# Optimization experiments

Measured on AMD Instinct MI355X. Metric: run time of the kernel, lower is better.

Reference implementation:

```python
import jax, jax.numpy as jnp
import numpy as np

B, N, C, D = 32, 4096, 16, 256

def setup_inputs() -> dict:
    key = jax.random.key(0)
    k1, k2 = jax.random.split(key)
    r_tensor = jax.random.uniform(k1, (B, N, C), dtype=jnp.float32)
    v_tensor = jax.random.normal(k2, (B, N, D), dtype=jnp.float32)
    return {"r_tensor": r_tensor, "v_tensor": v_tensor}

def reference(r_tensor, v_tensor):
    n = r_tensor.shape[1]
    mask_belong = r_tensor >= 0.5  # (B,N,C)
    # mean over N of v[:, :, None, :] * mask[..., None]  ==  mask^T @ v / N, no (B,N,C,D) intermediate
    interest_category_mean = jnp.einsum(
        'bnc,bnd->bcd', mask_belong.astype(v_tensor.dtype), v_tensor) / n  # (B,C,D)
    mask_all_below = jnp.logical_not(mask_belong).all(axis=2)  # (B,N)
    interest_special_mean = jnp.einsum(
        'bn,bnd->bd', mask_all_below.astype(v_tensor.dtype), v_tensor) / n  # (B,D)
    v_fusion = jnp.concatenate(
        [interest_category_mean, interest_special_mean[:, None, :]], axis=1)  # (B,C+1,D)
    v_fusion = jnp.where(jnp.isnan(v_fusion), jnp.zeros((), v_fusion.dtype), v_fusion)
    return v_fusion
```

## Files before the change

kernel.cpp:

```cpp
#include <hip/hip_runtime.h>

#define B_ 32
#define N_ 4096
#define C_ 16
#define D_ 256
#define NSPLIT 64
#define ROWS (N_ / NSPLIT)
#define RPW  (ROWS / 4)
#define NG   (RPW / 4)

__global__ __launch_bounds__(256, 4)
void tensor_fusion_kernel(const float* __restrict__ r,
                          const float* __restrict__ v,
                          float* __restrict__ out) {
    const int b     = blockIdx.x >> 6;
    const int chunk = blockIdx.x & (NSPLIT - 1);
    const int tid   = threadIdx.x;
    const int wave  = tid >> 6;
    const int lane  = tid & 63;
    const int d4    = lane << 2;

    const float* __restrict__ rb = r + (size_t)b * N_ * C_;
    const float* __restrict__ vp = v + (size_t)b * N_ * D_;
    const float scale = 1.0f / (float)N_;
    float* __restrict__ ob = out + (size_t)b * 17 * D_;

    float4 acc[16];
#pragma unroll
    for (int c = 0; c < 16; ++c) acc[c] = make_float4(0.f, 0.f, 0.f, 0.f);

    const int base = chunk * ROWS + wave * RPW;

    const float* __restrict__ rptr = rb + (size_t)base * C_ + lane;
    const float* __restrict__ vptr = vp + (size_t)base * D_ + d4;

    float  rv;
    float4 v0, v1, v2, v3;
    float  rv_n;
    float4 n0, n1, n2, n3;

#define LOADG(off, RV, A, Bq, Cq, Dq)                                   \
    {                                                                   \
        RV = rptr[(size_t)(off) * C_];                                  \
        const float* _vn = vptr + (size_t)(off) * D_;                   \
        A  = *(const float4*)(_vn + 0 * D_);                            \
        Bq = *(const float4*)(_vn + 1 * D_);                            \
        Cq = *(const float4*)(_vn + 2 * D_);                            \
        Dq = *(const float4*)(_vn + 3 * D_);                            \
    }

#define ACCROW(VV, MASK)                                                \
    {                                                                   \
        const unsigned _m = (MASK);                                     \
        _Pragma("unroll")                                               \
        for (int c = 0; c < 16; ++c) {                                  \
            const float m = (_m & (1u << c)) ? 1.0f : 0.0f;             \
            acc[c].x += (VV).x * m;                                     \
            acc[c].y += (VV).y * m;                                     \
            acc[c].z += (VV).z * m;                                     \
            acc[c].w += (VV).w * m;                                     \
        }                                                               \
        if (_m == 0u) {    \
            atomicAdd(&ob[16 * D_ + d4 + 0], (VV).x * scale);           \
            atomicAdd(&ob[16 * D_ + d4 + 1], (VV).y * scale);           \
            atomicAdd(&ob[16 * D_ + d4 + 2], (VV).z * scale);           \
            atomicAdd(&ob[16 * D_ + d4 + 3], (VV).w * scale);           \
        }                                                               \
    }

    LOADG(0, rv, v0, v1, v2, v3);

#pragma unroll
    for (int g = 0; g < NG; ++g) {
        if (g + 1 < NG) LOADG((g + 1) * 4, rv_n, n0, n1, n2, n3);

        const unsigned long long bal = __ballot(rv >= 0.5f);
        ACCROW(v0, (unsigned)(bal       ) & 0xFFFFu);
        ACCROW(v1, (unsigned)(bal >> 16 ) & 0xFFFFu);
        ACCROW(v2, (unsigned)(bal >> 32 ) & 0xFFFFu);
        ACCROW(v3, (unsigned)(bal >> 48 ) & 0xFFFFu);

        if (g + 1 < NG) { rv = rv_n; v0 = n0; v1 = n1; v2 = n2; v3 = n3; }
    }

    __shared__ float4 lds4[16 * 64];
    if (wave == 0) {
#pragma unroll
        for (int c = 0; c < 16; ++c) lds4[c * 64 + lane] = acc[c];
    }
    __syncthreads();
    for (int w = 1; w < 4; ++w) {
        if (wave == w) {
#pragma unroll
            for (int c = 0; c < 16; ++c) {
                float4 t = lds4[c * 64 + lane];
                t.x += acc[c].x; t.y += acc[c].y;
                t.z += acc[c].z; t.w += acc[c].w;
                lds4[c * 64 + lane] = t;
            }
        }
        __syncthreads();
    }

    const float* lf = (const float*)lds4;
#pragma unroll
    for (int c = 0; c < 16; ++c) {
        atomicAdd(&ob[c * D_ + tid], lf[c * 256 + tid] * scale);
    }
}

extern "C" void kernel_launch(void* const* d_in, const int* in_sizes, int n_in,
                              void* d_out, int out_size, void* d_ws, size_t ws_size,
                              hipStream_t stream) {
    const float* r = (const float*)d_in[0];
    const float* v = (const float*)d_in[1];
    float* out = (float*)d_out;

    hipMemsetAsync(out, 0, (size_t)out_size * sizeof(float), stream);

    dim3 grid(B_ * NSPLIT);
    tensor_fusion_kernel<<<grid, 256, 0, stream>>>(r, v, out);
}
```

Measured before the change: 203.4 us.

## Split D across wave pairs with float2 accumulators to cut registers

Each pair of waves now splits the 256-wide D dimension in halves with float2 loads and 16 float2 accumulators instead of float4, and two wave pairs each handle 32 rows of the 64-row chunk. This halves accumulator registers, permitting launch_bounds occupancy of 8 blocks per CU, and shrinks the cross-wave LDS reduction to a single add step with fewer barriers. The cost is redundant ballot/r loads per wave pair, narrower global loads, and twice as many per-element atomics for the special row.

```diff
diff --git a/kernel.cpp b/kernel.cpp
--- a/kernel.cpp
+++ b/kernel.cpp
@@ -5,11 +5,11 @@
 #define C_ 16
 #define D_ 256
 #define NSPLIT 64
-#define ROWS (N_ / NSPLIT)
-#define RPW  (ROWS / 4)
-#define NG   (RPW / 4)
+#define ROWS 64
+#define RPS  32
+#define NG   8
 
-__global__ __launch_bounds__(256, 4)
+__global__ __launch_bounds__(256, 8)
 void tensor_fusion_kernel(const float* __restrict__ r,
                           const float* __restrict__ v,
                           float* __restrict__ out) {
@@ -18,54 +18,49 @@
     const int tid   = threadIdx.x;
     const int wave  = tid >> 6;
     const int lane  = tid & 63;
-    const int d4    = lane << 2;
+    const int sub   = wave >> 1;
+    const int half  = wave & 1;
+    const int d2    = half * 128 + (lane << 1);
 
     const float* __restrict__ rb = r + (size_t)b * N_ * C_;
     const float* __restrict__ vp = v + (size_t)b * N_ * D_;
     const float scale = 1.0f / (float)N_;
     float* __restrict__ ob = out + (size_t)b * 17 * D_;
 
-    float4 acc[16];
+    float2 acc[16];
 #pragma unroll
-    for (int c = 0; c < 16; ++c) acc[c] = make_float4(0.f, 0.f, 0.f, 0.f);
+    for (int c = 0; c < 16; ++c) acc[c] = make_float2(0.f, 0.f);
 
-    const int base = chunk * ROWS + wave * RPW;
+    const int base = chunk * ROWS + sub * RPS;
+    const float* __restrict__ rptr = rb + (size_t)base * C_ + lane;
+    const float* __restrict__ vptr = vp + (size_t)base * D_ + d2;
 
-    const float* __restrict__ rptr = rb + (size_t)base * C_ + lane;
-    const float* __restrict__ vptr = vp + (size_t)base * D_ + d4;
+    float  rv, rv_n;
+    float2 v0, v1, v2, v3, n0, n1, n2, n3;
 
-    float  rv;
-    float4 v0, v1, v2, v3;
-    float  rv_n;
-    float4 n0, n1, n2, n3;
-
-#define LOADG(off, RV, A, Bq, Cq, Dq)                                   \
-    {                                                                   \
-        RV = rptr[(size_t)(off) * C_];                                  \
-        const float* _vn = vptr + (size_t)(off) * D_;                   \
-        A  = *(const float4*)(_vn + 0 * D_);                            \
-        Bq = *(const float4*)(_vn + 1 * D_);                            \
-        Cq = *(const float4*)(_vn + 2 * D_);                            \
-        Dq = *(const float4*)(_vn + 3 * D_);                            \
+#define LOADG(off, RV, A, Bq, Cq, Dq)                          \
+    {                                                          \
+        RV = rptr[(size_t)(off) * C_];                         \
+        const float* _vn = vptr + (size_t)(off) * D_;          \
+        A  = *(const float2*)(_vn + 0 * D_);                   \
+        Bq = *(const float2*)(_vn + 1 * D_);                   \
+        Cq = *(const float2*)(_vn + 2 * D_);                   \
+        Dq = *(const float2*)(_vn + 3 * D_);                   \
     }
 
-#define ACCROW(VV, MASK)                                                \
-    {                                                                   \
-        const unsigned _m = (MASK);                                     \
-        _Pragma("unroll")                                               \
-        for (int c = 0; c < 16; ++c) {                                  \
-            const float m = (_m & (1u << c)) ? 1.0f : 0.0f;             \
-            acc[c].x += (VV).x * m;                                     \
-            acc[c].y += (VV).y * m;                                     \
-            acc[c].z += (VV).z * m;                                     \
-            acc[c].w += (VV).w * m;                                     \
-        }                                                               \
-        if (_m == 0u) {    \
-            atomicAdd(&ob[16 * D_ + d4 + 0], (VV).x * scale);           \
-            atomicAdd(&ob[16 * D_ + d4 + 1], (VV).y * scale);           \
-            atomicAdd(&ob[16 * D_ + d4 + 2], (VV).z * scale);           \
-            atomicAdd(&ob[16 * D_ + d4 + 3], (VV).w * scale);           \
-        }                                                               \
+#define ACCROW(VV, MASK)                                       \
+    {                                                          \
+        const unsigned _m = (MASK);                            \
+        _Pragma("unroll")                                      \
+        for (int c = 0; c < 16; ++c) {                         \
+            const float m = (_m & (1u << c)) ? 1.0f : 0.0f;    \
+            acc[c].x += (VV).x * m;                            \
+            acc[c].y += (VV).y * m;                            \
+        }                                                      \
+        if (_m == 0u) {        \
+            atomicAdd(&ob[16 * D_ + d2 + 0], (VV).x * scale);  \
+            atomicAdd(&ob[16 * D_ + d2 + 1], (VV).y * scale);  \
+        }                                                      \
     }
 
     LOADG(0, rv, v0, v1, v2, v3);
@@ -83,26 +78,24 @@
         if (g + 1 < NG) { rv = rv_n; v0 = n0; v1 = n1; v2 = n2; v3 = n3; }
     }
 
-    __shared__ float4 lds4[16 * 64];
-    if (wave == 0) {
+    __shared__ float2 lds2[16 * 128];
+    const int li = half * 64 + lane;
+    if (sub == 0) {
 #pragma unroll
-        for (int c = 0; c < 16; ++c) lds4[c * 64 + lane] = acc[c];
+        for (int c = 0; c < 16; ++c) lds2[c * 128 + li] = acc[c];
     }
     __syncthreads();
-    for (int w = 1; w < 4; ++w) {
-        if (wave == w) {
+    if (sub == 1) {
 #pragma unroll
-            for (int c = 0; c < 16; ++c) {
-                float4 t = lds4[c * 64 + lane];
-                t.x += acc[c].x; t.y += acc[c].y;
-                t.z += acc[c].z; t.w += acc[c].w;
-                lds4[c * 64 + lane] = t;
-            }
+        for (int c = 0; c < 16; ++c) {
+            float2 t = lds2[c * 128 + li];
+            t.x += acc[c].x; t.y += acc[c].y;
+            lds2[c * 128 + li] = t;
         }
-        __syncthreads();
     }
+    __syncthreads();
 
-    const float* lf = (const float*)lds4;
+    const float* lf = (const float*)lds2;
 #pragma unroll
     for (int c = 0; c < 16; ++c) {
         atomicAdd(&ob[c * D_ + tid], lf[c * 256 + tid] * scale);
```

Result: slower. 236.3 us (+16.1%).
